# Kernel tuning notes

Measured on AMD Instinct MI355X. Metric: run time of the kernel, lower is better.

Reference implementation:

```python
import jax, jax.numpy as jnp
import numpy as np

NUM_SPECIES = 7
B, A, F = 1024, 48, 384


def setup_inputs() -> dict:
    key = jax.random.key(0)
    ks = jax.random.split(key, 10)
    species = jax.random.randint(ks[0], (B, A), 0, NUM_SPECIES, dtype=jnp.int32)
    aev = jax.random.normal(ks[1], (B, A, F), dtype=jnp.float32)
    def w(k, shape, fan_in):
        s = 1.0 / np.sqrt(fan_in).astype(np.float32)
        return jax.random.uniform(k, shape, jnp.float32, -s, s)
    return {
        "species": species,
        "aev": aev,
        "W1": w(ks[2], (NUM_SPECIES, 256, 384), 384),
        "b1": w(ks[3], (NUM_SPECIES, 256), 384),
        "W2": w(ks[4], (NUM_SPECIES, 192, 256), 256),
        "b2": w(ks[5], (NUM_SPECIES, 192), 256),
        "W3": w(ks[6], (NUM_SPECIES, 160, 192), 192),
        "b3": w(ks[7], (NUM_SPECIES, 160), 192),
        "W4": w(ks[8], (NUM_SPECIES, 1, 160), 160),
        "b4": w(ks[9], (NUM_SPECIES, 1), 160),
    }


def reference(species, aev, W1, b1, W2, b2, W3, b3, W4, b4):
    # species: [B, A] int, aev: [B, A, 384]
    celu = lambda x: jax.nn.celu(x, alpha=0.1)

    def expert(s):
        # Per-species MLP 384->256->192->160->1 applied to all atoms; selected via mask.
        h = celu(jnp.einsum('baf,hf->bah', aev, W1[s]) + b1[s])
        h = celu(jnp.einsum('bah,gh->bag', h, W2[s]) + b2[s])
        h = celu(jnp.einsum('bag,eg->bae', h, W3[s]) + b3[s])
        return (jnp.einsum('bae,oe->bao', h, W4[s]) + b4[s])[..., 0]  # [B, A]

    atom_energy = jnp.zeros(species.shape, aev.dtype)
    for s in range(NUM_SPECIES):  # fixed small expert loop (hard routing)
        atom_energy = jnp.where(species == s, expert(s), atom_energy)
    # scatter-sum atomic energies into per-molecule energies
    return atom_energy.sum(axis=1)  # [B]
```

## Files before the change

### kernel.cpp

```cpp
#include <hip/hip_runtime.h>
#include <math.h>

#define NSPEC 7
#define NMOL 1024
#define APM 48
#define NATOMS (NMOL * APM)
#define FDIM 384

typedef unsigned short u16;
typedef unsigned int u32;
typedef __attribute__((ext_vector_type(8))) short short8;
typedef __attribute__((ext_vector_type(4))) float floatx4;

#define W1_ELEMS_PER_S (16 * 12 * 64 * 8)
#define W2_ELEMS_PER_S (12 * 8 * 64 * 8)
#define W3_ELEMS_PER_S (10 * 6 * 64 * 8)
#define T1 (NSPEC * 16 * 12 * 64)
#define T2 (NSPEC * 12 * 8 * 64)
#define T3 (NSPEC * 10 * 6 * 64)
#define BUCKET_BLOCKS (NATOMS / 256)
#define PACK_BLOCKS ((T1 + T2 + T3) / 256)

#define WS_W1_OFF 32
#define WS_W2_OFF (WS_W1_OFF + 1376256)
#define WS_W3_OFF (WS_W2_OFF + 688128)
#define WS_BKT_OFF (WS_W3_OFF + 430080)

#define BUFST 264

__device__ __forceinline__ float celu01(float x) {
    return x > 0.0f ? x : 0.1f * expm1f(x * 10.0f);
}

__device__ __forceinline__ u16 bfr(float f) {
    u32 u = __float_as_uint(f);
    u += 0x7fffu + ((u >> 16) & 1u);
    return (u16)(u >> 16);
}

__device__ __forceinline__ float bf2f(short s) {
    return __uint_as_float(((u32)(u16)s) << 16);
}

union U8 { short8 v; u16 u[8]; };

__global__ void prep_kernel(const int* __restrict__ species,
                            int* __restrict__ g_cnt, u16* __restrict__ bucket,
                            const float* __restrict__ W1, const float* __restrict__ W2,
                            const float* __restrict__ W3,
                            u16* __restrict__ w1p, u16* __restrict__ w2p,
                            u16* __restrict__ w3p) {
    int t = threadIdx.x;
    if (blockIdx.x < BUCKET_BLOCKS) {
        __shared__ int l_cnt[NSPEC];
        __shared__ int l_base[NSPEC];
        if (t < NSPEC) l_cnt[t] = 0;
        __syncthreads();
        int i = blockIdx.x * 256 + t;
        int s = species[i];
        int lpos = atomicAdd(&l_cnt[s], 1);
        __syncthreads();
        if (t < NSPEC) l_base[t] = atomicAdd(&g_cnt[t], l_cnt[t]);
        __syncthreads();
        bucket[s * NATOMS + l_base[s] + lpos] = (u16)i;
    } else {
        int tid = (blockIdx.x - BUCKET_BLOCKS) * 256 + t;
        const float* W;
        u16* dst;
        int KGS, NTILES, idx;
        if (tid < T1) { W = W1; dst = w1p; KGS = 12; NTILES = 16; idx = tid; }
        else if (tid < T1 + T2) { W = W2; dst = w2p; KGS = 8; NTILES = 12; idx = tid - T1; }
        else { W = W3; dst = w3p; KGS = 6; NTILES = 10; idx = tid - (T1 + T2); }
        int lane = idx & 63;
        int q = idx >> 6;
        int kg = q % KGS; q /= KGS;
        int t2 = q % NTILES;
        int s = q / NTILES;
        int K = KGS * 32;
        int n = t2 * 16 + (lane & 15);
        int k0 = kg * 32 + ((lane >> 4) & 3) * 8;
        const float* src = W + (size_t)(s * NTILES * 16 + n) * K + k0;
        U8 x;
#pragma unroll
        for (int j = 0; j < 8; ++j) x.u[j] = bfr(src[j]);
        *reinterpret_cast<short8*>(dst + (size_t)idx * 8) = x.v;
    }
}

template <int KGS, int NTILES>
__device__ __forceinline__ void run_layer(const short8* af0, const short8* af1,
                                          const u16* __restrict__ wsp,
                                          const float* __restrict__ bias,
                                          u16* __restrict__ outbuf, int lane) {
    const int nl = lane & 15, kg4 = lane >> 4;
    short8 bcur[KGS], bnext[KGS];
    {
        const u16* wb = wsp + (size_t)lane * 8;
#pragma unroll
        for (int kg = 0; kg < KGS; ++kg)
            bcur[kg] = *reinterpret_cast<const short8*>(wb + kg * 512);
    }
#pragma unroll
    for (int t = 0; t < NTILES; ++t) {
        if (t + 1 < NTILES) {
            const u16* wb = wsp + (size_t)((t + 1) * KGS) * 512 + (size_t)lane * 8;
#pragma unroll
            for (int kg = 0; kg < KGS; ++kg)
                bnext[kg] = *reinterpret_cast<const short8*>(wb + kg * 512);
        }
        floatx4 acc0 = {0.f, 0.f, 0.f, 0.f};
        floatx4 acc1 = {0.f, 0.f, 0.f, 0.f};
#pragma unroll
        for (int kg = 0; kg < KGS; ++kg) {
            acc0 = __builtin_amdgcn_mfma_f32_16x16x32_bf16(af0[kg], bcur[kg], acc0, 0, 0, 0);
            acc1 = __builtin_amdgcn_mfma_f32_16x16x32_bf16(af1[kg], bcur[kg], acc1, 0, 0, 0);
        }
        float bn = bias[t * 16 + nl];
#pragma unroll
        for (int r = 0; r < 4; ++r) {
            outbuf[(kg4 * 4 + r) * BUFST + t * 16 + nl] = bfr(celu01(acc0[r] + bn));
            outbuf[(16 + kg4 * 4 + r) * BUFST + t * 16 + nl] = bfr(celu01(acc1[r] + bn));
        }
#pragma unroll
        for (int kg = 0; kg < KGS; ++kg) bcur[kg] = bnext[kg];
    }
}

template <int KGS>
__device__ __forceinline__ void load_a_lds(const u16* __restrict__ buf,
                                           short8* af0, short8* af1, int lane) {
    int nl = lane & 15, kg4 = lane >> 4;
#pragma unroll
    for (int kg = 0; kg < KGS; ++kg) {
        af0[kg] = *reinterpret_cast<const short8*>(buf + (size_t)nl * BUFST + kg * 32 + kg4 * 8);
        af1[kg] = *reinterpret_cast<const short8*>(buf + (size_t)(16 + nl) * BUFST + kg * 32 + kg4 * 8);
    }
}

__global__ __launch_bounds__(128, 2) void mlp_kernel(
    const float* __restrict__ aev,
    const u16* __restrict__ w1p, const u16* __restrict__ w2p, const u16* __restrict__ w3p,
    const float* __restrict__ b1, const float* __restrict__ b2, const float* __restrict__ b3,
    const float* __restrict__ W4, const float* __restrict__ b4,
    const int* __restrict__ g_cnt, const u16* __restrict__ bucket,
    float* __restrict__ out) {
    int s = blockIdx.y;
    int cnt = g_cnt[s];
    int w = threadIdx.x >> 6, lane = threadIdx.x & 63;
    int base = blockIdx.x * 64 + w * 32;
    if (base >= cnt) return;

    __shared__ __align__(16) u16 bufs[2][32 * BUFST];
    u16* buf = &bufs[w][0];

    int nl = lane & 15, kg4 = lane >> 4;

    short8 af0[12], af1[12];
    {
        int i0 = base + nl;       if (i0 >= cnt) i0 = cnt - 1;
        int i1 = base + 16 + nl;  if (i1 >= cnt) i1 = cnt - 1;
        int a0 = (int)bucket[s * NATOMS + i0];
        int a1 = (int)bucket[s * NATOMS + i1];
        const float* ar0 = aev + (size_t)a0 * FDIM;
        const float* ar1 = aev + (size_t)a1 * FDIM;
#pragma unroll
        for (int kg = 0; kg < 12; ++kg) {
            const float4* p0 = (const float4*)(ar0 + kg * 32 + kg4 * 8);
            const float4* p1 = (const float4*)(ar1 + kg * 32 + kg4 * 8);
            float4 a = p0[0], b = p0[1];
            float4 c = p1[0], d = p1[1];
            U8 x, y;
            x.u[0] = bfr(a.x); x.u[1] = bfr(a.y); x.u[2] = bfr(a.z); x.u[3] = bfr(a.w);
            x.u[4] = bfr(b.x); x.u[5] = bfr(b.y); x.u[6] = bfr(b.z); x.u[7] = bfr(b.w);
            y.u[0] = bfr(c.x); y.u[1] = bfr(c.y); y.u[2] = bfr(c.z); y.u[3] = bfr(c.w);
            y.u[4] = bfr(d.x); y.u[5] = bfr(d.y); y.u[6] = bfr(d.z); y.u[7] = bfr(d.w);
            af0[kg] = x.v;
            af1[kg] = y.v;
        }
    }
    run_layer<12, 16>(af0, af1, w1p + (size_t)s * W1_ELEMS_PER_S, b1 + s * 256, buf, lane);

    short8 c0[8], c1[8];
    load_a_lds<8>(buf, c0, c1, lane);
    run_layer<8, 12>(c0, c1, w2p + (size_t)s * W2_ELEMS_PER_S, b2 + s * 192, buf, lane);

    short8 d0[6], d1[6];
    load_a_lds<6>(buf, d0, d1, lane);
    run_layer<6, 10>(d0, d1, w3p + (size_t)s * W3_ELEMS_PER_S, b3 + s * 160, buf, lane);

    {
        int m = lane >> 1, q = lane & 1;
        const u16* h = buf + (size_t)m * BUFST + q * 80;
        const float* w4s = W4 + s * 160 + q * 80;
        float p = 0.f;
#pragma unroll
        for (int c = 0; c < 10; ++c) {
            short8 hv = *reinterpret_cast<const short8*>(h + c * 8);
            const float4* wp4 = (const float4*)(w4s + c * 8);
            float4 wa = wp4[0], wb = wp4[1];
            p += bf2f(hv[0]) * wa.x + bf2f(hv[1]) * wa.y + bf2f(hv[2]) * wa.z + bf2f(hv[3]) * wa.w;
            p += bf2f(hv[4]) * wb.x + bf2f(hv[5]) * wb.y + bf2f(hv[6]) * wb.z + bf2f(hv[7]) * wb.w;
        }
        p += __shfl_down(p, 1, 2);
        int idx = base + m;
        if (q == 0 && idx < cnt) {
            int atom = (int)bucket[s * NATOMS + idx];
            atomicAdd(&out[atom / APM], p + b4[s]);
        }
    }
}

extern "C" void kernel_launch(void* const* d_in, const int* in_sizes, int n_in,
                              void* d_out, int out_size, void* d_ws, size_t ws_size,
                              hipStream_t stream) {
    const int* species = (const int*)d_in[0];
    const float* aev = (const float*)d_in[1];
    const float* W1 = (const float*)d_in[2];
    const float* b1 = (const float*)d_in[3];
    const float* W2 = (const float*)d_in[4];
    const float* b2 = (const float*)d_in[5];
    const float* W3 = (const float*)d_in[6];
    const float* b3 = (const float*)d_in[7];
    const float* W4 = (const float*)d_in[8];
    const float* b4 = (const float*)d_in[9];
    float* out = (float*)d_out;

    unsigned char* wsb = (unsigned char*)d_ws;
    int* g_cnt = (int*)wsb;
    u16* w1p = (u16*)(wsb + WS_W1_OFF);
    u16* w2p = (u16*)(wsb + WS_W2_OFF);
    u16* w3p = (u16*)(wsb + WS_W3_OFF);
    u16* bucket = (u16*)(wsb + WS_BKT_OFF);

    hipMemsetAsync(d_out, 0, NMOL * sizeof(float), stream);
    hipMemsetAsync(g_cnt, 0, 8 * sizeof(int), stream);

    prep_kernel<<<BUCKET_BLOCKS + PACK_BLOCKS, 256, 0, stream>>>(
        species, g_cnt, bucket, W1, W2, W3, w1p, w2p, w3p);

    dim3 grid(NATOMS / 64, NSPEC);
    mlp_kernel<<<grid, 128, 0, stream>>>(aev, w1p, w2p, w3p, b1, b2, b3, W4, b4,
                                         g_cnt, bucket, out);
}
```

Measured before the change: 193.4 us.

## Split each layer's output columns across two waves sharing one atom tile

Each block now handles 32 atoms, and its two waves each compute half of every layer's output columns into a shared LDS buffer, with barriers between layers. Before, each wave ran a separate 32-atom tile over all columns. This halves the weight bytes each wave streams and doubles the grid, aiming to cut weight-load traffic per atom and add parallelism. The cost is extra __syncthreads and duplicated activation loads. It also replaces expm1f with a __expf-based CELU, vectorizes the weight packing loads, folds the output memset into prep_kernel, and raises launch bounds to 3 blocks per CU.

```diff
diff --git a/kernel.cpp b/kernel.cpp
--- a/kernel.cpp
+++ b/kernel.cpp
@@ -29,7 +29,8 @@
 #define BUFST 264
 
 __device__ __forceinline__ float celu01(float x) {
-    return x > 0.0f ? x : 0.1f * expm1f(x * 10.0f);
+    float e = fmaf(0.1f, __expf(x * 10.0f), -0.1f);
+    return x > 0.0f ? x : e;
 }
 
 __device__ __forceinline__ u16 bfr(float f) {
@@ -43,20 +44,44 @@
 }
 
 union U8 { short8 v; u16 u[8]; };
+
+template <int KGS, int NTILES>
+__device__ __forceinline__ void pack_w(const float* __restrict__ W,
+                                       u16* __restrict__ dst, int idx) {
+    int lane = idx & 63;
+    int q = idx >> 6;
+    int kg = q % KGS; q /= KGS;
+    int t2 = q % NTILES;
+    int s = q / NTILES;
+    const int K = KGS * 32;
+    int n = t2 * 16 + (lane & 15);
+    int k0 = kg * 32 + ((lane >> 4) & 3) * 8;
+    const float4* src = (const float4*)(W + (size_t)(s * NTILES * 16 + n) * K + k0);
+    float4 a = src[0], b = src[1];
+    U8 x;
+    x.u[0] = bfr(a.x); x.u[1] = bfr(a.y); x.u[2] = bfr(a.z); x.u[3] = bfr(a.w);
+    x.u[4] = bfr(b.x); x.u[5] = bfr(b.y); x.u[6] = bfr(b.z); x.u[7] = bfr(b.w);
+    *reinterpret_cast<short8*>(dst + (size_t)idx * 8) = x.v;
+}
 
 __global__ void prep_kernel(const int* __restrict__ species,
                             int* __restrict__ g_cnt, u16* __restrict__ bucket,
                             const float* __restrict__ W1, const float* __restrict__ W2,
                             const float* __restrict__ W3,
                             u16* __restrict__ w1p, u16* __restrict__ w2p,
-                            u16* __restrict__ w3p) {
+                            u16* __restrict__ w3p, float* __restrict__ out) {
     int t = threadIdx.x;
-    if (blockIdx.x < BUCKET_BLOCKS) {
+    int bx = blockIdx.x;
+    if (bx < BUCKET_BLOCKS) {
+        if (bx == 0) {
+            float4 z = {0.f, 0.f, 0.f, 0.f};
+            ((float4*)out)[t] = z;
+        }
         __shared__ int l_cnt[NSPEC];
         __shared__ int l_base[NSPEC];
         if (t < NSPEC) l_cnt[t] = 0;
         __syncthreads();
-        int i = blockIdx.x * 256 + t;
+        int i = bx * 256 + t;
         int s = species[i];
         int lpos = atomicAdd(&l_cnt[s], 1);
         __syncthreads();
@@ -64,49 +89,32 @@
         __syncthreads();
         bucket[s * NATOMS + l_base[s] + lpos] = (u16)i;
     } else {
-        int tid = (blockIdx.x - BUCKET_BLOCKS) * 256 + t;
-        const float* W;
-        u16* dst;
-        int KGS, NTILES, idx;
-        if (tid < T1) { W = W1; dst = w1p; KGS = 12; NTILES = 16; idx = tid; }
-        else if (tid < T1 + T2) { W = W2; dst = w2p; KGS = 8; NTILES = 12; idx = tid - T1; }
-        else { W = W3; dst = w3p; KGS = 6; NTILES = 10; idx = tid - (T1 + T2); }
-        int lane = idx & 63;
-        int q = idx >> 6;
-        int kg = q % KGS; q /= KGS;
-        int t2 = q % NTILES;
-        int s = q / NTILES;
-        int K = KGS * 32;
-        int n = t2 * 16 + (lane & 15);
-        int k0 = kg * 32 + ((lane >> 4) & 3) * 8;
-        const float* src = W + (size_t)(s * NTILES * 16 + n) * K + k0;
-        U8 x;
-#pragma unroll
-        for (int j = 0; j < 8; ++j) x.u[j] = bfr(src[j]);
-        *reinterpret_cast<short8*>(dst + (size_t)idx * 8) = x.v;
-    }
-}
-
-template <int KGS, int NTILES>
+        int tid = (bx - BUCKET_BLOCKS) * 256 + t;
+        if (tid < T1) pack_w<12, 16>(W1, w1p, tid);
+        else if (tid < T1 + T2) pack_w<8, 12>(W2, w2p, tid - T1);
+        else pack_w<6, 10>(W3, w3p, tid - (T1 + T2));
+    }
+}
+
+template <int KGS, int NT>
 __device__ __forceinline__ void run_layer(const short8* af0, const short8* af1,
                                           const u16* __restrict__ wsp,
                                           const float* __restrict__ bias,
-                                          u16* __restrict__ outbuf, int lane) {
+                                          u16* __restrict__ outbuf,
+                                          int lane, int colbase) {
     const int nl = lane & 15, kg4 = lane >> 4;
     short8 bcur[KGS], bnext[KGS];
-    {
-        const u16* wb = wsp + (size_t)lane * 8;
-#pragma unroll
-        for (int kg = 0; kg < KGS; ++kg)
-            bcur[kg] = *reinterpret_cast<const short8*>(wb + kg * 512);
-    }
-#pragma unroll
-    for (int t = 0; t < NTILES; ++t) {
-        if (t + 1 < NTILES) {
-            const u16* wb = wsp + (size_t)((t + 1) * KGS) * 512 + (size_t)lane * 8;
+    const u16* wb = wsp + (size_t)lane * 8;
+#pragma unroll
+    for (int kg = 0; kg < KGS; ++kg)
+        bcur[kg] = *reinterpret_cast<const short8*>(wb + kg * 512);
+#pragma unroll
+    for (int t = 0; t < NT; ++t) {
+        if (t + 1 < NT) {
+            const u16* wn = wb + (size_t)(t + 1) * (KGS * 512);
 #pragma unroll
             for (int kg = 0; kg < KGS; ++kg)
-                bnext[kg] = *reinterpret_cast<const short8*>(wb + kg * 512);
+                bnext[kg] = *reinterpret_cast<const short8*>(wn + kg * 512);
         }
         floatx4 acc0 = {0.f, 0.f, 0.f, 0.f};
         floatx4 acc1 = {0.f, 0.f, 0.f, 0.f};
@@ -116,10 +124,11 @@
             acc1 = __builtin_amdgcn_mfma_f32_16x16x32_bf16(af1[kg], bcur[kg], acc1, 0, 0, 0);
         }
         float bn = bias[t * 16 + nl];
+        int col = colbase + t * 16 + nl;
 #pragma unroll
         for (int r = 0; r < 4; ++r) {
-            outbuf[(kg4 * 4 + r) * BUFST + t * 16 + nl] = bfr(celu01(acc0[r] + bn));
-            outbuf[(16 + kg4 * 4 + r) * BUFST + t * 16 + nl] = bfr(celu01(acc1[r] + bn));
+            outbuf[(kg4 * 4 + r) * BUFST + col] = bfr(celu01(acc0[r] + bn));
+            outbuf[(16 + kg4 * 4 + r) * BUFST + col] = bfr(celu01(acc1[r] + bn));
         }
 #pragma unroll
         for (int kg = 0; kg < KGS; ++kg) bcur[kg] = bnext[kg];
@@ -137,7 +146,7 @@
     }
 }
 
-__global__ __launch_bounds__(128, 2) void mlp_kernel(
+__global__ __launch_bounds__(128, 3) void mlp_kernel(
     const float* __restrict__ aev,
     const u16* __restrict__ w1p, const u16* __restrict__ w2p, const u16* __restrict__ w3p,
     const float* __restrict__ b1, const float* __restrict__ b2, const float* __restrict__ b3,
@@ -146,13 +155,12 @@
     float* __restrict__ out) {
     int s = blockIdx.y;
     int cnt = g_cnt[s];
+    int base = blockIdx.x * 32;
+    if (base >= cnt) return;
+
+    __shared__ __align__(16) u16 buf[32 * BUFST];
+
     int w = threadIdx.x >> 6, lane = threadIdx.x & 63;
-    int base = blockIdx.x * 64 + w * 32;
-    if (base >= cnt) return;
-
-    __shared__ __align__(16) u16 bufs[2][32 * BUFST];
-    u16* buf = &bufs[w][0];
-
     int nl = lane & 15, kg4 = lane >> 4;
 
     short8 af0[12], af1[12];
@@ -178,30 +186,43 @@
             af1[kg] = y.v;
         }
     }
-    run_layer<12, 16>(af0, af1, w1p + (size_t)s * W1_ELEMS_PER_S, b1 + s * 256, buf, lane);
+
+    run_layer<12, 8>(af0, af1,
+                     w1p + (size_t)s * W1_ELEMS_PER_S + (size_t)w * (8 * 12 * 512),
+                     b1 + s * 256 + w * 128, buf, lane, w * 128);
+    __syncthreads();
 
     short8 c0[8], c1[8];
     load_a_lds<8>(buf, c0, c1, lane);
-    run_layer<8, 12>(c0, c1, w2p + (size_t)s * W2_ELEMS_PER_S, b2 + s * 192, buf, lane);
+    __syncthreads();
+    run_layer<8, 6>(c0, c1,
+                    w2p + (size_t)s * W2_ELEMS_PER_S + (size_t)w * (6 * 8 * 512),
+                    b2 + s * 192 + w * 96, buf, lane, w * 96);
+    __syncthreads();
 
     short8 d0[6], d1[6];
     load_a_lds<6>(buf, d0, d1, lane);
-    run_layer<6, 10>(d0, d1, w3p + (size_t)s * W3_ELEMS_PER_S, b3 + s * 160, buf, lane);
+    __syncthreads();
+    run_layer<6, 5>(d0, d1,
+                    w3p + (size_t)s * W3_ELEMS_PER_S + (size_t)w * (5 * 6 * 512),
+                    b3 + s * 160 + w * 80, buf, lane, w * 80);
+    __syncthreads();
 
     {
-        int m = lane >> 1, q = lane & 1;
-        const u16* h = buf + (size_t)m * BUFST + q * 80;
-        const float* w4s = W4 + s * 160 + q * 80;
+        int m = w * 16 + (lane >> 2), q = lane & 3;
+        const u16* h = buf + (size_t)m * BUFST + q * 40;
+        const float* w4s = W4 + s * 160 + q * 40;
         float p = 0.f;
 #pragma unroll
-        for (int c = 0; c < 10; ++c) {
+        for (int c = 0; c < 5; ++c) {
             short8 hv = *reinterpret_cast<const short8*>(h + c * 8);
             const float4* wp4 = (const float4*)(w4s + c * 8);
             float4 wa = wp4[0], wb = wp4[1];
             p += bf2f(hv[0]) * wa.x + bf2f(hv[1]) * wa.y + bf2f(hv[2]) * wa.z + bf2f(hv[3]) * wa.w;
             p += bf2f(hv[4]) * wb.x + bf2f(hv[5]) * wb.y + bf2f(hv[6]) * wb.z + bf2f(hv[7]) * wb.w;
         }
-        p += __shfl_down(p, 1, 2);
+        p += __shfl_down(p, 2, 4);
+        p += __shfl_down(p, 1, 4);
         int idx = base + m;
         if (q == 0 && idx < cnt) {
             int atom = (int)bucket[s * NATOMS + idx];
@@ -232,13 +253,12 @@
     u16* w3p = (u16*)(wsb + WS_W3_OFF);
     u16* bucket = (u16*)(wsb + WS_BKT_OFF);
 
-    hipMemsetAsync(d_out, 0, NMOL * sizeof(float), stream);
     hipMemsetAsync(g_cnt, 0, 8 * sizeof(int), stream);
 
     prep_kernel<<<BUCKET_BLOCKS + PACK_BLOCKS, 256, 0, stream>>>(
-        species, g_cnt, bucket, W1, W2, W3, w1p, w2p, w3p);
-
-    dim3 grid(NATOMS / 64, NSPEC);
+        species, g_cnt, bucket, W1, W2, W3, w1p, w2p, w3p, out);
+
+    dim3 grid(NATOMS / 32, NSPEC);
     mlp_kernel<<<grid, 128, 0, stream>>>(aev, w1p, w2p, w3p, b1, b2, b3, W4, b4,
                                          g_cnt, bucket, out);
 }
```

Result: slower. 209.6 us (+8.4%).
